# Kernel optimization log

Hardware: AMD Instinct MI355X
Metric: run time of the kernel (lower is better)

Reference implementation:

```python
import jax, jax.numpy as jnp
import numpy as np

N_NODES = 50000
N_EDGES = 800000
IN_C, HID_C, OUT_C = 256, 256, 128


def gcn_conv(x, W, b, row, col, n_nodes):
    """PyG GCNConv: linear transform, symmetric-normalized aggregation, bias.
    row/col already include self-loops. Messages flow row -> col."""
    h = x @ W  # [N, out]
    deg = jax.ops.segment_sum(jnp.ones_like(col, dtype=h.dtype), col, num_segments=n_nodes)
    d_inv_sqrt = jnp.where(deg > 0, jax.lax.rsqrt(jnp.maximum(deg, 1e-12)), 0.0)
    norm = d_inv_sqrt[row] * d_inv_sqrt[col]  # [E]
    msg = h[row] * norm[:, None]              # gather + scale, [E, out]
    out = jax.ops.segment_sum(msg, col, num_segments=n_nodes)  # scatter-add
    return out + b


def setup_inputs() -> dict:
    key = jax.random.key(0)
    k_x, k_e, k_w1, k_w2 = jax.random.split(key, 4)
    x = jax.random.normal(k_x, (N_NODES, IN_C), dtype=jnp.float32)
    edge_index = jax.random.randint(k_e, (2, N_EDGES), 0, N_NODES, dtype=jnp.int64)
    # Glorot-style init for GCN weights, zeros bias (PyG default)
    s1 = float(np.sqrt(6.0 / (IN_C + HID_C)))
    s2 = float(np.sqrt(6.0 / (HID_C + OUT_C)))
    W1 = jax.random.uniform(k_w1, (IN_C, HID_C), dtype=jnp.float32, minval=-s1, maxval=s1)
    b1 = jnp.zeros((HID_C,), dtype=jnp.float32)
    W2 = jax.random.uniform(k_w2, (HID_C, OUT_C), dtype=jnp.float32, minval=-s2, maxval=s2)
    b2 = jnp.zeros((OUT_C,), dtype=jnp.float32)
    return {"x": x, "edge_index": edge_index, "W1": W1, "b1": b1, "W2": W2, "b2": b2}


def reference(x, edge_index, W1, b1, W2, b2):
    n = x.shape[0]
    # add self-loops (PyG GCNConv default add_self_loops=True)
    loops = jnp.arange(n, dtype=edge_index.dtype)
    row = jnp.concatenate([edge_index[0], loops])
    col = jnp.concatenate([edge_index[1], loops])
    h = gcn_conv(x, W1, b1, row, col, n)
    h = jax.nn.relu(h)  # dropout p=0.0 -> identity
    out = gcn_conv(h, W2, b2, row, col, n)
    return out
```

## Files before the change

kernel.cpp:

```cpp
#include <hip/hip_runtime.h>

#define NN 50000
#define NE 800000
#define IN_C 256
#define HID_C 256
#define OUT_C 128

typedef unsigned short u16;
typedef __attribute__((ext_vector_type(8))) short short8;
typedef __attribute__((ext_vector_type(8))) unsigned short ushort8;
typedef __attribute__((ext_vector_type(4))) float f32x4;

__device__ __forceinline__ u16 f2b(float f) {
  unsigned int u = __float_as_uint(f);
  return (u16)((u + 0x7FFFu + ((u >> 16) & 1u)) >> 16);
}
__device__ __forceinline__ float b2f(u16 s) {
  return __uint_as_float(((unsigned int)s) << 16);
}


__global__ __launch_bounds__(256) void hist_kernel(const int* __restrict__ col,
                                                   int* __restrict__ cnt, int E) {
  int e = blockIdx.x * blockDim.x + threadIdx.x;
  if (e < E) atomicAdd(&cnt[col[e]], 1);
}

__global__ __launch_bounds__(256) void scan1_kernel(const int* __restrict__ cnt,
                                                    int* __restrict__ bsum, int n) {
  __shared__ int ws[4];
  int i = blockIdx.x * 256 + threadIdx.x;
  int lane = threadIdx.x & 63, wid = threadIdx.x >> 6;
  int v = (i < n) ? cnt[i] : 0;
#pragma unroll
  for (int off = 32; off > 0; off >>= 1) v += __shfl_down(v, off, 64);
  if (lane == 0) ws[wid] = v;
  __syncthreads();
  if (threadIdx.x == 0) bsum[blockIdx.x] = ws[0] + ws[1] + ws[2] + ws[3];
}

__global__ __launch_bounds__(256) void scan2_kernel(const int* __restrict__ bsum,
                                                    int* __restrict__ boff,
                                                    int* __restrict__ row_off,
                                                    int nb, int n) {
  __shared__ int wsum[4], wpre[5];
  int lane = threadIdx.x & 63, wid = threadIdx.x >> 6;
  int v = (threadIdx.x < nb) ? bsum[threadIdx.x] : 0;
  int s = v;
#pragma unroll
  for (int off = 1; off < 64; off <<= 1) {
    int t = __shfl_up(s, off, 64);
    if (lane >= off) s += t;
  }
  if (lane == 63) wsum[wid] = s;
  __syncthreads();
  if (threadIdx.x == 0) {
    int acc = 0;
#pragma unroll
    for (int w = 0; w < 4; ++w) { wpre[w] = acc; acc += wsum[w]; }
    wpre[4] = acc;
  }
  __syncthreads();
  if (threadIdx.x < nb) boff[threadIdx.x] = wpre[wid] + (s - v);
  if (threadIdx.x == 0) row_off[n] = wpre[4];
}

__global__ __launch_bounds__(256) void scan3_kernel(const int* __restrict__ cnt,
                                                    const int* __restrict__ boff,
                                                    int* __restrict__ row_off,
                                                    int* __restrict__ cursor,
                                                    float* __restrict__ dinv, int n) {
  __shared__ int wsum[4], wpre[4];
  int i = blockIdx.x * 256 + threadIdx.x;
  int lane = threadIdx.x & 63, wid = threadIdx.x >> 6;
  int v = (i < n) ? cnt[i] : 0;
  int s = v;
#pragma unroll
  for (int off = 1; off < 64; off <<= 1) {
    int t = __shfl_up(s, off, 64);
    if (lane >= off) s += t;
  }
  if (lane == 63) wsum[wid] = s;
  __syncthreads();
  if (threadIdx.x == 0) {
    int acc = 0;
#pragma unroll
    for (int w = 0; w < 4; ++w) { wpre[w] = acc; acc += wsum[w]; }
  }
  __syncthreads();
  if (i < n) {
    int off = boff[blockIdx.x] + wpre[wid] + (s - v);
    row_off[i] = off;
    cursor[i] = off;
    dinv[i] = rsqrtf((float)(v + 1));
  }
}

__global__ __launch_bounds__(256) void scatter_kernel(const int* __restrict__ row,
                                                      const int* __restrict__ col,
                                                      int* __restrict__ cursor,
                                                      int* __restrict__ csr, int E) {
  int e = blockIdx.x * blockDim.x + threadIdx.x;
  if (e < E) {
    int c = col[e];
    int p = atomicAdd(&cursor[c], 1);
    csr[p] = row[e];
  }
}


__global__ __launch_bounds__(256) void convw_kernel(const float* __restrict__ W1,
                                                    const float* __restrict__ W2,
                                                    u16* __restrict__ W1t,
                                                    u16* __restrict__ W2t) {
  int id = blockIdx.x * 256 + threadIdx.x;
  if (id < 256 * 256) {
    int n = id >> 8, k = id & 255;
    W1t[id] = f2b(W1[k * 256 + n]);
  }
  if (id < 128 * 256) {
    int n = id >> 8, k = id & 255;
    W2t[id] = f2b(W2[k * 128 + n]);
  }
}


template <bool A_IS_F32>
__global__ __launch_bounds__(256) void gemm_mfma(const void* __restrict__ Ap,
                                                 const u16* __restrict__ Bt,
                                                 const float* __restrict__ dscale,
                                                 u16* __restrict__ C, int M, int N) {
  __shared__ u16 Asl[2][128 * 40];
  __shared__ u16 Bsl[2][128 * 40];
  const int tid = threadIdx.x;
  const int row0 = blockIdx.y * 128;
  const int col0 = blockIdx.x * 128;

  f32x4 acc[4][4] = {};

  const int seg = tid & 7;
  const int rb = tid >> 3;
  const int wave = tid >> 6, lane = tid & 63;
  const int wm = wave >> 1, wn = wave & 1;
  const int qr = lane & 15, quad = lane >> 4;

  float4 aF[4];
  ushort4 aU[4];
  ushort4 bR[4];

  auto load_tiles = [&](int k0) {
    if constexpr (A_IS_F32) {
      const float* A = (const float*)Ap;
#pragma unroll
      for (int i = 0; i < 4; ++i) {
        int gr = row0 + rb + i * 32;
        aF[i] = (gr < M) ? *(const float4*)&A[(size_t)gr * 256 + k0 + seg * 4]
                         : make_float4(0.f, 0.f, 0.f, 0.f);
      }
    } else {
      const u16* A = (const u16*)Ap;
#pragma unroll
      for (int i = 0; i < 4; ++i) {
        int gr = row0 + rb + i * 32;
        aU[i] = (gr < M) ? *(const ushort4*)&A[(size_t)gr * 256 + k0 + seg * 4]
                         : make_ushort4(0, 0, 0, 0);
      }
    }
#pragma unroll
    for (int i = 0; i < 4; ++i) {
      int n = rb + i * 32;
      bR[i] = *(const ushort4*)&Bt[(size_t)(col0 + n) * 256 + k0 + seg * 4];
    }
  };

  auto write_lds = [&](int buf) {
#pragma unroll
    for (int i = 0; i < 4; ++i) {
      int r = rb + i * 32;
      ushort4 u;
      if constexpr (A_IS_F32) {
        u.x = f2b(aF[i].x); u.y = f2b(aF[i].y);
        u.z = f2b(aF[i].z); u.w = f2b(aF[i].w);
      } else {
        u = aU[i];
      }
      *(ushort4*)&Asl[buf][r * 40 + seg * 4] = u;
      *(ushort4*)&Bsl[buf][r * 40 + seg * 4] = bR[i];
    }
  };

  load_tiles(0);
  write_lds(0);
  __syncthreads();

#pragma unroll
  for (int it = 0; it < 8; ++it) {
    const int cur = it & 1;
    if (it < 7) load_tiles((it + 1) * 32);

    short8 afr[4], bfr[4];
#pragma unroll
    for (int mt = 0; mt < 4; ++mt)
      afr[mt] = *(const short8*)&Asl[cur][(wm * 64 + mt * 16 + qr) * 40 + quad * 8];
#pragma unroll
    for (int nt = 0; nt < 4; ++nt)
      bfr[nt] = *(const short8*)&Bsl[cur][(wn * 64 + nt * 16 + qr) * 40 + quad * 8];
#pragma unroll
    for (int mt = 0; mt < 4; ++mt)
#pragma unroll
      for (int nt = 0; nt < 4; ++nt)
        acc[mt][nt] = __builtin_amdgcn_mfma_f32_16x16x32_bf16(afr[mt], bfr[nt], acc[mt][nt], 0, 0, 0);

    if (it < 7) {
      write_lds(1 - cur);
      __syncthreads();
    }
  }

#pragma unroll
  for (int mt = 0; mt < 4; ++mt) {
#pragma unroll
    for (int i = 0; i < 4; ++i) {
      int gr = row0 + wm * 64 + mt * 16 + quad * 4 + i;
      if (gr < M) {
        float sc = dscale[gr];
#pragma unroll
        for (int nt = 0; nt < 4; ++nt) {
          int gc = col0 + wn * 64 + nt * 16 + qr;
          C[(size_t)gr * N + gc] = f2b(acc[mt][nt][i] * sc);
        }
      }
    }
  }
}


__global__ __launch_bounds__(256) void agg256_bf(const u16* __restrict__ h,
                                                 const int* __restrict__ row_off,
                                                 const int* __restrict__ csr,
                                                 const float* __restrict__ dinv,
                                                 const float* __restrict__ bias,
                                                 u16* __restrict__ out, int n) {
  int wave = threadIdx.x >> 6;
  int lane = threadIdx.x & 63;
  int half = lane >> 5;
  int sl = lane & 31;
  int v = blockIdx.x * 8 + wave * 2 + half;
  if (v >= n) return;
  int beg = row_off[v], end = row_off[v + 1];
  float a[8] = {};
  int e = beg;
  for (; e + 7 < end; e += 8) {
    int s[8];
#pragma unroll
    for (int j = 0; j < 8; ++j) s[j] = csr[e + j];
    ushort8 g[8];
#pragma unroll
    for (int j = 0; j < 8; ++j)
      g[j] = *(const ushort8*)&h[(size_t)s[j] * 256 + sl * 8];
#pragma unroll
    for (int j = 0; j < 8; ++j)
#pragma unroll
      for (int i = 0; i < 8; ++i) a[i] += b2f((u16)g[j][i]);
  }
  for (; e + 1 < end; e += 2) {
    int s0 = csr[e], s1 = csr[e + 1];
    ushort8 g0 = *(const ushort8*)&h[(size_t)s0 * 256 + sl * 8];
    ushort8 g1 = *(const ushort8*)&h[(size_t)s1 * 256 + sl * 8];
#pragma unroll
    for (int i = 0; i < 8; ++i) a[i] += b2f((u16)g0[i]) + b2f((u16)g1[i]);
  }
  if (e < end) {
    int s0 = csr[e];
    ushort8 g0 = *(const ushort8*)&h[(size_t)s0 * 256 + sl * 8];
#pragma unroll
    for (int i = 0; i < 8; ++i) a[i] += b2f((u16)g0[i]);
  }
  ushort8 hs = *(const ushort8*)&h[(size_t)v * 256 + sl * 8];
#pragma unroll
  for (int i = 0; i < 8; ++i) a[i] += b2f((u16)hs[i]);
  float dv = dinv[v];
  float4 bv0 = *(const float4*)&bias[sl * 8];
  float4 bv1 = *(const float4*)&bias[sl * 8 + 4];
  float bb[8] = {bv0.x, bv0.y, bv0.z, bv0.w, bv1.x, bv1.y, bv1.z, bv1.w};
  ushort8 o;
#pragma unroll
  for (int i = 0; i < 8; ++i) {
    float r = fmaxf(a[i] * dv + bb[i], 0.f);
    o[i] = (short)f2b(r);
  }
  *(ushort8*)&out[(size_t)v * 256 + sl * 8] = o;
}

__global__ __launch_bounds__(256) void agg128_bf(const u16* __restrict__ h,
                                                 const int* __restrict__ row_off,
                                                 const int* __restrict__ csr,
                                                 const float* __restrict__ dinv,
                                                 const float* __restrict__ bias,
                                                 float* __restrict__ out, int n) {
  int wave = threadIdx.x >> 6;
  int lane = threadIdx.x & 63;
  int quarter = lane >> 4;
  int sl = lane & 15;
  int v = blockIdx.x * 16 + wave * 4 + quarter;
  if (v >= n) return;
  int beg = row_off[v], end = row_off[v + 1];
  float a[8] = {};
  int e = beg;
  for (; e + 7 < end; e += 8) {
    int s[8];
#pragma unroll
    for (int j = 0; j < 8; ++j) s[j] = csr[e + j];
    ushort8 g[8];
#pragma unroll
    for (int j = 0; j < 8; ++j)
      g[j] = *(const ushort8*)&h[(size_t)s[j] * 128 + sl * 8];
#pragma unroll
    for (int j = 0; j < 8; ++j)
#pragma unroll
      for (int i = 0; i < 8; ++i) a[i] += b2f((u16)g[j][i]);
  }
  for (; e + 1 < end; e += 2) {
    int s0 = csr[e], s1 = csr[e + 1];
    ushort8 g0 = *(const ushort8*)&h[(size_t)s0 * 128 + sl * 8];
    ushort8 g1 = *(const ushort8*)&h[(size_t)s1 * 128 + sl * 8];
#pragma unroll
    for (int i = 0; i < 8; ++i) a[i] += b2f((u16)g0[i]) + b2f((u16)g1[i]);
  }
  if (e < end) {
    int s0 = csr[e];
    ushort8 g0 = *(const ushort8*)&h[(size_t)s0 * 128 + sl * 8];
#pragma unroll
    for (int i = 0; i < 8; ++i) a[i] += b2f((u16)g0[i]);
  }
  ushort8 hs = *(const ushort8*)&h[(size_t)v * 128 + sl * 8];
#pragma unroll
  for (int i = 0; i < 8; ++i) a[i] += b2f((u16)hs[i]);
  float dv = dinv[v];
  float4 bv0 = *(const float4*)&bias[sl * 8];
  float4 bv1 = *(const float4*)&bias[sl * 8 + 4];
  float bb[8] = {bv0.x, bv0.y, bv0.z, bv0.w, bv1.x, bv1.y, bv1.z, bv1.w};
  float o[8];
#pragma unroll
  for (int i = 0; i < 8; ++i) o[i] = a[i] * dv + bb[i];
  *(float4*)&out[(size_t)v * 128 + sl * 8] = make_float4(o[0], o[1], o[2], o[3]);
  *(float4*)&out[(size_t)v * 128 + sl * 8 + 4] = make_float4(o[4], o[5], o[6], o[7]);
}


extern "C" void kernel_launch(void* const* d_in, const int* in_sizes, int n_in,
                              void* d_out, int out_size, void* d_ws, size_t ws_size,
                              hipStream_t stream) {
  const float* x = (const float*)d_in[0];
  const int* ei = (const int*)d_in[1];
  const float* W1 = (const float*)d_in[2];
  const float* b1 = (const float*)d_in[3];
  const float* W2 = (const float*)d_in[4];
  const float* b2 = (const float*)d_in[5];
  float* out = (float*)d_out;

  const int* row = ei;
  const int* col = ei + NE;

  const int NB = (NN + 255) / 256;

  u16* Hb = (u16*)d_ws;
  u16* H2b = Hb + (size_t)NN * 256;
  u16* H3b = H2b + (size_t)NN * 256;
  u16* W1t = H3b + (size_t)NN * 128;
  u16* W2t = W1t + 256 * 256;
  int* cnt = (int*)(W2t + 128 * 256);
  int* row_off = cnt + NN;
  int* cursor = row_off + NN + 1;
  float* dinv = (float*)(cursor + NN);
  int* bsum = (int*)(dinv + NN);
  int* boff = bsum + NB;
  int* csr = boff + NB;

  hipMemsetAsync(cnt, 0, NN * sizeof(int), stream);
  convw_kernel<<<256, 256, 0, stream>>>(W1, W2, W1t, W2t);
  hist_kernel<<<(NE + 255) / 256, 256, 0, stream>>>(col, cnt, NE);
  scan1_kernel<<<NB, 256, 0, stream>>>(cnt, bsum, NN);
  scan2_kernel<<<1, 256, 0, stream>>>(bsum, boff, row_off, NB, NN);
  scan3_kernel<<<NB, 256, 0, stream>>>(cnt, boff, row_off, cursor, dinv, NN);
  scatter_kernel<<<(NE + 255) / 256, 256, 0, stream>>>(row, col, cursor, csr, NE);

  {
    dim3 grid(HID_C / 128, (NN + 127) / 128);
    gemm_mfma<true><<<grid, 256, 0, stream>>>(x, W1t, dinv, Hb, NN, HID_C);
  }
  agg256_bf<<<(NN + 7) / 8, 256, 0, stream>>>(Hb, row_off, csr, dinv, b1, H2b, NN);

  {
    dim3 grid(OUT_C / 128, (NN + 127) / 128);
    gemm_mfma<false><<<grid, 256, 0, stream>>>(H2b, W2t, dinv, H3b, NN, OUT_C);
  }
  agg128_bf<<<(NN + 15) / 16, 256, 0, stream>>>(H3b, row_off, csr, dinv, b2, out, NN);
}
```

Baseline: 316.7 us.

## Fuse CSR scatter into first GEMM launch, merge memset, vectorize index loads

Moves the edge-to-CSR scatter work into extra blocks of the first GEMM launch so the atomic scatter can overlap with the dense transform. The memset is folded into the weight-conversion kernel, which removes launches. The aggregation kernels now load CSR indices as aligned int4 after a short alignment prologue, and the workspace offsets are padded for alignment. The fused launch uses the GEMM's shared-memory footprint for every block, including the scatter blocks, which can reduce occupancy for them.

```diff
diff --git a/kernel.cpp b/kernel.cpp
--- a/kernel.cpp
+++ b/kernel.cpp
@@ -17,6 +17,29 @@
 }
 __device__ __forceinline__ float b2f(u16 s) {
   return __uint_as_float(((unsigned int)s) << 16);
+}
+
+
+__global__ __launch_bounds__(256) void convw_zero(const float* __restrict__ W1,
+                                                  const float* __restrict__ W2,
+                                                  u16* __restrict__ W1t,
+                                                  u16* __restrict__ W2t,
+                                                  int* __restrict__ cnt) {
+  int b = blockIdx.x;
+  if (b < 256) {
+    int id = b * 256 + threadIdx.x;
+    if (id < 256 * 256) {
+      int n = id >> 8, k = id & 255;
+      W1t[id] = f2b(W1[k * 256 + n]);
+    }
+    if (id < 128 * 256) {
+      int n = id >> 8, k = id & 255;
+      W2t[id] = f2b(W2[k * 128 + n]);
+    }
+  } else {
+    int i = (b - 256) * 256 + threadIdx.x;
+    if (i < NN) cnt[i] = 0;
+  }
 }
 
 
@@ -96,45 +119,17 @@
   }
 }
 
-__global__ __launch_bounds__(256) void scatter_kernel(const int* __restrict__ row,
-                                                      const int* __restrict__ col,
-                                                      int* __restrict__ cursor,
-                                                      int* __restrict__ csr, int E) {
-  int e = blockIdx.x * blockDim.x + threadIdx.x;
-  if (e < E) {
-    int c = col[e];
-    int p = atomicAdd(&cursor[c], 1);
-    csr[p] = row[e];
-  }
-}
-
-
-__global__ __launch_bounds__(256) void convw_kernel(const float* __restrict__ W1,
-                                                    const float* __restrict__ W2,
-                                                    u16* __restrict__ W1t,
-                                                    u16* __restrict__ W2t) {
-  int id = blockIdx.x * 256 + threadIdx.x;
-  if (id < 256 * 256) {
-    int n = id >> 8, k = id & 255;
-    W1t[id] = f2b(W1[k * 256 + n]);
-  }
-  if (id < 128 * 256) {
-    int n = id >> 8, k = id & 255;
-    W2t[id] = f2b(W2[k * 128 + n]);
-  }
-}
-
 
 template <bool A_IS_F32>
-__global__ __launch_bounds__(256) void gemm_mfma(const void* __restrict__ Ap,
-                                                 const u16* __restrict__ Bt,
-                                                 const float* __restrict__ dscale,
-                                                 u16* __restrict__ C, int M, int N) {
-  __shared__ u16 Asl[2][128 * 40];
-  __shared__ u16 Bsl[2][128 * 40];
+__device__ __forceinline__ void gemm_body(const void* __restrict__ Ap,
+                                          const u16* __restrict__ Bt,
+                                          const float* __restrict__ dscale,
+                                          u16* __restrict__ C, int M, int N,
+                                          int bx, int by,
+                                          u16 (&Asl)[2][5120], u16 (&Bsl)[2][5120]) {
   const int tid = threadIdx.x;
-  const int row0 = blockIdx.y * 128;
-  const int col0 = blockIdx.x * 128;
+  const int row0 = by * 128;
+  const int col0 = bx * 128;
 
   f32x4 acc[4][4] = {};
 
@@ -230,6 +225,40 @@
           C[(size_t)gr * N + gc] = f2b(acc[mt][nt][i] * sc);
         }
       }
+    }
+  }
+}
+
+template <bool A_IS_F32>
+__global__ __launch_bounds__(256) void gemm_mfma(const void* __restrict__ Ap,
+                                                 const u16* __restrict__ Bt,
+                                                 const float* __restrict__ dscale,
+                                                 u16* __restrict__ C, int M, int N) {
+  __shared__ u16 Asl[2][5120];
+  __shared__ u16 Bsl[2][5120];
+  gemm_body<A_IS_F32>(Ap, Bt, dscale, C, M, N, blockIdx.x, blockIdx.y, Asl, Bsl);
+}
+
+__global__ __launch_bounds__(256) void gemm1_scatter(const float* __restrict__ x,
+                                                     const u16* __restrict__ W1t,
+                                                     const float* __restrict__ dinv,
+                                                     u16* __restrict__ Hb, int M, int N,
+                                                     int ngb,
+                                                     const int* __restrict__ row,
+                                                     const int* __restrict__ col,
+                                                     int* __restrict__ cursor,
+                                                     int* __restrict__ csr, int E) {
+  __shared__ u16 Asl[2][5120];
+  __shared__ u16 Bsl[2][5120];
+  int b = blockIdx.x;
+  if (b < ngb) {
+    gemm_body<true>(x, W1t, dinv, Hb, M, N, b & 1, b >> 1, Asl, Bsl);
+  } else {
+    int e = (b - ngb) * 256 + threadIdx.x;
+    if (e < E) {
+      int c = col[e];
+      int p = atomicAdd(&cursor[c], 1);
+      csr[p] = row[e];
     }
   }
 }
@@ -250,10 +279,16 @@
   int beg = row_off[v], end = row_off[v + 1];
   float a[8] = {};
   int e = beg;
+  for (; e < end && (e & 3); ++e) {
+    int s0 = csr[e];
+    ushort8 g0 = *(const ushort8*)&h[(size_t)s0 * 256 + sl * 8];
+#pragma unroll
+    for (int i = 0; i < 8; ++i) a[i] += b2f((u16)g0[i]);
+  }
   for (; e + 7 < end; e += 8) {
-    int s[8];
-#pragma unroll
-    for (int j = 0; j < 8; ++j) s[j] = csr[e + j];
+    int4 i0 = *(const int4*)&csr[e];
+    int4 i1 = *(const int4*)&csr[e + 4];
+    int s[8] = {i0.x, i0.y, i0.z, i0.w, i1.x, i1.y, i1.z, i1.w};
     ushort8 g[8];
 #pragma unroll
     for (int j = 0; j < 8; ++j)
@@ -263,14 +298,7 @@
 #pragma unroll
       for (int i = 0; i < 8; ++i) a[i] += b2f((u16)g[j][i]);
   }
-  for (; e + 1 < end; e += 2) {
-    int s0 = csr[e], s1 = csr[e + 1];
-    ushort8 g0 = *(const ushort8*)&h[(size_t)s0 * 256 + sl * 8];
-    ushort8 g1 = *(const ushort8*)&h[(size_t)s1 * 256 + sl * 8];
-#pragma unroll
-    for (int i = 0; i < 8; ++i) a[i] += b2f((u16)g0[i]) + b2f((u16)g1[i]);
-  }
-  if (e < end) {
+  for (; e < end; ++e) {
     int s0 = csr[e];
     ushort8 g0 = *(const ushort8*)&h[(size_t)s0 * 256 + sl * 8];
 #pragma unroll
@@ -307,10 +335,16 @@
   int beg = row_off[v], end = row_off[v + 1];
   float a[8] = {};
   int e = beg;
+  for (; e < end && (e & 3); ++e) {
+    int s0 = csr[e];
+    ushort8 g0 = *(const ushort8*)&h[(size_t)s0 * 128 + sl * 8];
+#pragma unroll
+    for (int i = 0; i < 8; ++i) a[i] += b2f((u16)g0[i]);
+  }
   for (; e + 7 < end; e += 8) {
-    int s[8];
-#pragma unroll
-    for (int j = 0; j < 8; ++j) s[j] = csr[e + j];
+    int4 i0 = *(const int4*)&csr[e];
+    int4 i1 = *(const int4*)&csr[e + 4];
+    int s[8] = {i0.x, i0.y, i0.z, i0.w, i1.x, i1.y, i1.z, i1.w};
     ushort8 g[8];
 #pragma unroll
     for (int j = 0; j < 8; ++j)
@@ -320,14 +354,7 @@
 #pragma unroll
       for (int i = 0; i < 8; ++i) a[i] += b2f((u16)g[j][i]);
   }
-  for (; e + 1 < end; e += 2) {
-    int s0 = csr[e], s1 = csr[e + 1];
-    ushort8 g0 = *(const ushort8*)&h[(size_t)s0 * 128 + sl * 8];
-    ushort8 g1 = *(const ushort8*)&h[(size_t)s1 * 128 + sl * 8];
-#pragma unroll
-    for (int i = 0; i < 8; ++i) a[i] += b2f((u16)g0[i]) + b2f((u16)g1[i]);
-  }
-  if (e < end) {
+  for (; e < end; ++e) {
     int s0 = csr[e];
     ushort8 g0 = *(const ushort8*)&h[(size_t)s0 * 128 + sl * 8];
 #pragma unroll
@@ -371,23 +398,23 @@
   u16* W2t = W1t + 256 * 256;
   int* cnt = (int*)(W2t + 128 * 256);
   int* row_off = cnt + NN;
-  int* cursor = row_off + NN + 1;
+  int* cursor = row_off + NN + 4;
   float* dinv = (float*)(cursor + NN);
   int* bsum = (int*)(dinv + NN);
-  int* boff = bsum + NB;
-  int* csr = boff + NB;
-
-  hipMemsetAsync(cnt, 0, NN * sizeof(int), stream);
-  convw_kernel<<<256, 256, 0, stream>>>(W1, W2, W1t, W2t);
+  int* boff = bsum + 200;
+  int* csr = boff + 200;
+
+  convw_zero<<<256 + NB, 256, 0, stream>>>(W1, W2, W1t, W2t, cnt);
   hist_kernel<<<(NE + 255) / 256, 256, 0, stream>>>(col, cnt, NE);
   scan1_kernel<<<NB, 256, 0, stream>>>(cnt, bsum, NN);
   scan2_kernel<<<1, 256, 0, stream>>>(bsum, boff, row_off, NB, NN);
   scan3_kernel<<<NB, 256, 0, stream>>>(cnt, boff, row_off, cursor, dinv, NN);
-  scatter_kernel<<<(NE + 255) / 256, 256, 0, stream>>>(row, col, cursor, csr, NE);
 
   {
-    dim3 grid(HID_C / 128, (NN + 127) / 128);
-    gemm_mfma<true><<<grid, 256, 0, stream>>>(x, W1t, dinv, Hb, NN, HID_C);
+    const int ngb = (HID_C / 128) * ((NN + 127) / 128);
+    const int nsb = (NE + 255) / 256;
+    gemm1_scatter<<<ngb + nsb, 256, 0, stream>>>(x, W1t, dinv, Hb, NN, HID_C, ngb,
+                                                 row, col, cursor, csr, NE);
   }
   agg256_bf<<<(NN + 7) / 8, 256, 0, stream>>>(Hb, row_off, csr, dinv, b1, H2b, NN);
 
```

Result: faster. 303.6 us (-4.1%).
